# Performance work log

Hardware: AMD Instinct MI355X
Metric: run time of the kernel (lower is better)

Reference implementation:

```python
import jax, jax.numpy as jnp
import numpy as np

B, D, NH, NT = 4096, 2048, 16, 4
DK = D // NH
EPS = 1e-5


def setup_inputs() -> dict:
    key = jax.random.key(0)
    ks = jax.random.split(key, 16)
    s = 0.02
    inp = {
        "e0": jax.random.normal(ks[0], (B, D), jnp.float32),
        "e1": jax.random.normal(ks[1], (B, D), jnp.float32),
        "e2": jax.random.normal(ks[2], (B, D), jnp.float32),
        "e3": jax.random.normal(ks[3], (B, D), jnp.float32),
        "quality": jax.random.uniform(ks[4], (B, NT), jnp.float32),
        "Wq": jax.random.normal(ks[5], (D, D), jnp.float32) * s,
        "bq": jnp.zeros((D,), jnp.float32),
        "Wk": jax.random.normal(ks[6], (D, D), jnp.float32) * s,
        "bk": jnp.zeros((D,), jnp.float32),
        "Wv": jax.random.normal(ks[7], (D, D), jnp.float32) * s,
        "bv": jnp.zeros((D,), jnp.float32),
        "Wo": jax.random.normal(ks[8], (D, D), jnp.float32) * s,
        "bo": jnp.zeros((D,), jnp.float32),
        "gamma": jnp.ones((D,), jnp.float32),
        "beta": jnp.zeros((D,), jnp.float32),
    }
    return inp


def _layer_norm(x, gamma, beta):
    mu = jnp.mean(x, axis=-1, keepdims=True)
    var = jnp.mean(jnp.square(x - mu), axis=-1, keepdims=True)
    return (x - mu) * jax.lax.rsqrt(var + EPS) * gamma + beta


def reference(e0, e1, e2, e3, quality, Wq, bq, Wk, bk, Wv, bv, Wo, bo, gamma, beta):
    # H: (B, T=4, D) stacked evidence representations
    H = jnp.stack([e0, e1, e2, e3], axis=1)
    # QKV projections, reshaped to (B, heads, T, dk)
    def proj(W, b):
        return (jnp.einsum('btd,ed->bte', H, W) + b).reshape(B, NT, NH, DK).transpose(0, 2, 1, 3)
    Q, K, V = proj(Wq, bq), proj(Wk, bk), proj(Wv, bv)
    # scores: (B, heads, Tq, Tk), scaled then multiplicatively quality-gated on keys
    scores = jnp.einsum('bhid,bhjd->bhij', Q, K) / jnp.sqrt(jnp.float32(DK))
    scores = scores * quality[:, None, None, :]
    attn = jax.nn.softmax(scores, axis=-1)  # dropout = identity at inference
    ctx = jnp.einsum('bhij,bhjd->bhid', attn, V)          # (B, H, T, dk)
    ctx = ctx.transpose(0, 2, 1, 3).reshape(B, NT, D)      # (B, T, D)
    ctx = jnp.einsum('btd,ed->bte', ctx, Wo) + bo
    fused = jnp.mean(ctx, axis=1)       # mean over evidence types
    residual = jnp.mean(H, axis=1)      # mean of ALL evidence types
    return _layer_norm(fused + residual, gamma, beta)
```

## Files before the change

### kernel.cpp

```cpp
#include <hip/hip_runtime.h>
#include <cstdint>
#include <cstddef>

#define BB 4096
#define DD 2048
#define NHH 16
#define NTT 4
#define DKK 128

using u16 = unsigned short;
using u32 = unsigned int;

typedef __bf16 bf16x8 __attribute__((ext_vector_type(8)));
typedef float f32x4 __attribute__((ext_vector_type(4)));

__device__ __forceinline__ float b2f(u16 u) {
    union { float f; u32 i; } c; c.i = ((u32)u) << 16; return c.f;
}
__device__ __forceinline__ u16 f2b(float f) {
    union { float f; u32 i; } c; c.f = f;
    u32 x = c.i;
    u32 r = (x + 0x7fffu + ((x >> 16) & 1u)) >> 16;
    return (u16)r;
}
__device__ __forceinline__ u32 pk(float lo, float hi) {
    u32 a = __builtin_bit_cast(u32, lo) + 0x8000u;
    u32 b = __builtin_bit_cast(u32, hi) + 0x8000u;
    return __builtin_amdgcn_perm(b, a, 0x07060302u);
}

__device__ __forceinline__ void load_lds16(const void* g, void* l) {
    __builtin_amdgcn_global_load_lds((const __attribute__((address_space(1))) void*)g,
                                     (__attribute__((address_space(3))) void*)l,
                                     16, 0, 0);
}

__global__ __launch_bounds__(256) void cvt_all(
    const float* __restrict__ e0, const float* __restrict__ e1,
    const float* __restrict__ e2, const float* __restrict__ e3,
    const float* __restrict__ Wq, const float* __restrict__ Wk,
    const float* __restrict__ Wv, const float* __restrict__ Wo,
    u16* __restrict__ Ebf, u16* __restrict__ W4, float* __restrict__ resid)
{
    const int blk = blockIdx.x;
    const int tid = threadIdx.x;
    if (blk < 4096) {
        const int b = blk;
        const int c = tid * 8;
        const size_t rb = (size_t)b * DD + c;
        const float* eps[4] = {e0, e1, e2, e3};
        float a8[8] = {0, 0, 0, 0, 0, 0, 0, 0};
#pragma unroll
        for (int t = 0; t < 4; ++t) {
            float4 p0 = *(const float4*)(eps[t] + rb);
            float4 p1 = *(const float4*)(eps[t] + rb + 4);
            u16* dst = Ebf + ((size_t)(b * 4 + t)) * DD + c;
            *(uint4*)dst = make_uint4(pk(p0.x, p0.y), pk(p0.z, p0.w),
                                      pk(p1.x, p1.y), pk(p1.z, p1.w));
            a8[0] += p0.x; a8[1] += p0.y; a8[2] += p0.z; a8[3] += p0.w;
            a8[4] += p1.x; a8[5] += p1.y; a8[6] += p1.z; a8[7] += p1.w;
        }
        *(float4*)(resid + rb)     = make_float4(a8[0] * 0.25f, a8[1] * 0.25f,
                                                 a8[2] * 0.25f, a8[3] * 0.25f);
        *(float4*)(resid + rb + 4) = make_float4(a8[4] * 0.25f, a8[5] * 0.25f,
                                                 a8[6] * 0.25f, a8[7] * 0.25f);
    } else {
        const int wb = blk - 4096;
        const int w = wb >> 11;
        const float* src = (w == 0) ? Wq : (w == 1) ? Wk : (w == 2) ? Wv : Wo;
        u16* dst = W4 + (size_t)w * DD * DD;
        const size_t i = (size_t)(wb & 2047) * 2048 + tid * 8;
        float4 a = *(const float4*)(src + i);
        float4 c2 = *(const float4*)(src + i + 4);
        *(uint4*)(dst + i) = make_uint4(pk(a.x, a.y), pk(a.z, a.w),
                                        pk(c2.x, c2.y), pk(c2.z, c2.w));
    }
}

__global__ __launch_bounds__(256, 2) void qkv_attn(
    const u16* __restrict__ Ebf,
    const u16* __restrict__ Wqb, const u16* __restrict__ Wkb,
    const u16* __restrict__ Wvb,
    const float* __restrict__ bq, const float* __restrict__ bk,
    const float* __restrict__ bv, const float* __restrict__ qual,
    u16* __restrict__ ctx)
{
    __shared__ __align__(16) u16 As [128 * 64];
    __shared__ __align__(16) u16 BQs[128 * 64];
    __shared__ __align__(16) u16 BKs[128 * 64];
    __shared__ __align__(16) u16 BVs[128 * 64];
    __shared__ float exch[4][4][4][16];

    const int tid = threadIdx.x;
    const int h = blockIdx.x;
    const int m0 = blockIdx.y * 128;
    const int n0 = h * 128;

    const int wave = tid >> 6;
    const int lane = tid & 63;

    const int srow = wave * 8 + (lane >> 3);
    const int scol = ((lane & 7) ^ (lane >> 3)) * 8;
    const u16* srcA = Ebf + (size_t)(m0 + srow) * DD + scol;
    const u16* srcQ = Wqb + (size_t)(n0 + srow) * DD + scol;
    const u16* srcK = Wkb + (size_t)(n0 + srow) * DD + scol;
    const u16* srcV = Wvb + (size_t)(n0 + srow) * DD + scol;

    char* ldsA = (char*)As  + wave * 1024;
    char* ldsQ = (char*)BQs + wave * 1024;
    char* ldsK = (char*)BKs + wave * 1024;
    char* ldsV = (char*)BVs + wave * 1024;

    const int lrow = lane & 15;
    const int q4 = lane >> 4;
    const int wm = (wave >> 1) * 64;
    const int wn = (wave & 1) * 64;
    const int soff0 = (q4 ^ (lrow & 7)) * 16;

    f32x4 aQ[4][4] = {};
    f32x4 aK[4][4] = {};
    f32x4 aV[4][4] = {};

    for (int k0 = 0; k0 < DD; k0 += 64) {
        __syncthreads();
#pragma unroll
        for (int i = 0; i < 4; ++i) {
            const size_t go = (size_t)i * 32 * DD;
            load_lds16(srcA + go, ldsA + i * 4096);
            load_lds16(srcQ + go, ldsQ + i * 4096);
            load_lds16(srcK + go, ldsK + i * 4096);
            load_lds16(srcV + go, ldsV + i * 4096);
        }
        srcA += 64; srcQ += 64; srcK += 64; srcV += 64;
        __syncthreads();

#pragma unroll
        for (int kk = 0; kk < 2; ++kk) {
            const int so = soff0 ^ (kk * 64);
            bf16x8 af[4];
#pragma unroll
            for (int mi = 0; mi < 4; ++mi)
                af[mi] = *(const bf16x8*)((const char*)As + (wm + mi * 16 + lrow) * 128 + so);
            {
                bf16x8 b4[4];
#pragma unroll
                for (int ni = 0; ni < 4; ++ni)
                    b4[ni] = *(const bf16x8*)((const char*)BQs + (wn + ni * 16 + lrow) * 128 + so);
#pragma unroll
                for (int mi = 0; mi < 4; ++mi)
#pragma unroll
                    for (int ni = 0; ni < 4; ++ni)
                        aQ[mi][ni] = __builtin_amdgcn_mfma_f32_16x16x32_bf16(af[mi], b4[ni], aQ[mi][ni], 0, 0, 0);
            }
            __builtin_amdgcn_sched_barrier(0);
            {
                bf16x8 b4[4];
#pragma unroll
                for (int ni = 0; ni < 4; ++ni)
                    b4[ni] = *(const bf16x8*)((const char*)BKs + (wn + ni * 16 + lrow) * 128 + so);
#pragma unroll
                for (int mi = 0; mi < 4; ++mi)
#pragma unroll
                    for (int ni = 0; ni < 4; ++ni)
                        aK[mi][ni] = __builtin_amdgcn_mfma_f32_16x16x32_bf16(af[mi], b4[ni], aK[mi][ni], 0, 0, 0);
            }
            __builtin_amdgcn_sched_barrier(0);
            {
                bf16x8 b4[4];
#pragma unroll
                for (int ni = 0; ni < 4; ++ni)
                    b4[ni] = *(const bf16x8*)((const char*)BVs + (wn + ni * 16 + lrow) * 128 + so);
#pragma unroll
                for (int mi = 0; mi < 4; ++mi)
#pragma unroll
                    for (int ni = 0; ni < 4; ++ni)
                        aV[mi][ni] = __builtin_amdgcn_mfma_f32_16x16x32_bf16(af[mi], b4[ni], aV[mi][ni], 0, 0, 0);
            }
            __builtin_amdgcn_sched_barrier(0);
        }
    }

    const int quad = lane >> 4;
    const int lcol = lane & 15;

    float qb[4], kb[4], vb[4];
#pragma unroll
    for (int ni = 0; ni < 4; ++ni) {
        const int col = n0 + wn + ni * 16 + lcol;
        qb[ni] = bq[col]; kb[ni] = bk[col]; vb[ni] = bv[col];
    }

#pragma unroll
    for (int mi = 0; mi < 4; ++mi) {
        float ps[4][4];
#pragma unroll
        for (int t = 0; t < 4; ++t)
#pragma unroll
            for (int j = 0; j < 4; ++j) ps[t][j] = 0.f;

#pragma unroll
        for (int ni = 0; ni < 4; ++ni) {
            float qv[4], kv[4];
#pragma unroll
            for (int t = 0; t < 4; ++t) {
                qv[t] = aQ[mi][ni][t] + qb[ni];
                kv[t] = aK[mi][ni][t] + kb[ni];
            }
#pragma unroll
            for (int t = 0; t < 4; ++t)
#pragma unroll
                for (int j = 0; j < 4; ++j) ps[t][j] += qv[t] * kv[j];
        }
#pragma unroll
        for (int t = 0; t < 4; ++t)
#pragma unroll
            for (int j = 0; j < 4; ++j) {
                ps[t][j] += __shfl_xor(ps[t][j], 1);
                ps[t][j] += __shfl_xor(ps[t][j], 2);
                ps[t][j] += __shfl_xor(ps[t][j], 4);
                ps[t][j] += __shfl_xor(ps[t][j], 8);
            }
        if (lcol == 0) {
#pragma unroll
            for (int t = 0; t < 4; ++t)
#pragma unroll
                for (int j = 0; j < 4; ++j)
                    exch[wave][mi][quad][t * 4 + j] = ps[t][j];
        }
    }
    __syncthreads();

    const float scale = 0.08838834764831845f;
#pragma unroll
    for (int mi = 0; mi < 4; ++mi) {
        const int bbat = (m0 >> 2) + (wave >> 1) * 16 + mi * 4 + quad;

        float s16[16];
#pragma unroll
        for (int v = 0; v < 16; ++v)
            s16[v] = exch[wave][mi][quad][v] + exch[wave ^ 1][mi][quad][v];

        float qj[4];
#pragma unroll
        for (int j = 0; j < 4; ++j) qj[j] = qual[bbat * 4 + j] * scale;

        float wsum[4] = {0.f, 0.f, 0.f, 0.f};
#pragma unroll
        for (int t = 0; t < 4; ++t) {
            float sm[4]; float mx = -1e30f;
#pragma unroll
            for (int j = 0; j < 4; ++j) { sm[j] = s16[t * 4 + j] * qj[j]; mx = fmaxf(mx, sm[j]); }
            float ex[4]; float se = 0.f;
#pragma unroll
            for (int j = 0; j < 4; ++j) { ex[j] = __expf(sm[j] - mx); se += ex[j]; }
            const float inv = 0.25f / se;
#pragma unroll
            for (int j = 0; j < 4; ++j) wsum[j] += ex[j] * inv;
        }

#pragma unroll
        for (int ni = 0; ni < 4; ++ni) {
            const int col = n0 + wn + ni * 16 + lcol;
            float r = wsum[0] * aV[mi][ni][0] + wsum[1] * aV[mi][ni][1]
                    + wsum[2] * aV[mi][ni][2] + wsum[3] * aV[mi][ni][3] + vb[ni];
            ctx[(size_t)bbat * DD + col] = f2b(r);
        }
    }
}

__global__ __launch_bounds__(256) void o_gemm(
    const u16* __restrict__ A, const u16* __restrict__ W,
    const float* __restrict__ bia, float* __restrict__ Y)
{
    __shared__ __align__(16) u16 As[128 * 64];
    __shared__ __align__(16) u16 Bs[128 * 64];

    const int tid = threadIdx.x;
    const int m0 = blockIdx.x * 128;
    const int n0 = blockIdx.y * 128;

    const int wave = tid >> 6;
    const int lane = tid & 63;

    const int srow = wave * 8 + (lane >> 3);
    const int scol = ((lane & 7) ^ (lane >> 3)) * 8;
    const u16* srcA = A + (size_t)(m0 + srow) * DD + scol;
    const u16* srcB = W + (size_t)(n0 + srow) * DD + scol;

    char* ldsA = (char*)As + wave * 1024;
    char* ldsB = (char*)Bs + wave * 1024;

    const int wm = (wave >> 1) * 64;
    const int wn = (wave & 1) * 64;
    const int lrow = lane & 15;
    const int q4 = lane >> 4;
    const int soff0 = (q4 ^ (lrow & 7)) * 16;

    f32x4 acc[4][4] = {};

    for (int k0 = 0; k0 < DD; k0 += 64) {
        __syncthreads();
#pragma unroll
        for (int i = 0; i < 4; ++i) {
            const size_t go = (size_t)i * 32 * DD;
            load_lds16(srcA + go, ldsA + i * 4096);
            load_lds16(srcB + go, ldsB + i * 4096);
        }
        srcA += 64; srcB += 64;
        __syncthreads();

#pragma unroll
        for (int kk = 0; kk < 2; ++kk) {
            const int so = soff0 ^ (kk * 64);
            bf16x8 af[4], bfr[4];
#pragma unroll
            for (int i = 0; i < 4; ++i)
                af[i] = *(const bf16x8*)((const char*)As + (wm + i * 16 + lrow) * 128 + so);
#pragma unroll
            for (int i = 0; i < 4; ++i)
                bfr[i] = *(const bf16x8*)((const char*)Bs + (wn + i * 16 + lrow) * 128 + so);
#pragma unroll
            for (int mi = 0; mi < 4; ++mi)
#pragma unroll
                for (int ni = 0; ni < 4; ++ni)
                    acc[mi][ni] = __builtin_amdgcn_mfma_f32_16x16x32_bf16(af[mi], bfr[ni], acc[mi][ni], 0, 0, 0);
        }
    }

#pragma unroll
    for (int mi = 0; mi < 4; ++mi) {
#pragma unroll
        for (int r = 0; r < 4; ++r) {
            const int grow = m0 + wm + mi * 16 + (lane >> 4) * 4 + r;
#pragma unroll
            for (int ni = 0; ni < 4; ++ni) {
                const int gcol = n0 + wn + ni * 16 + (lane & 15);
                Y[(size_t)grow * DD + gcol] = acc[mi][ni][r] + bia[gcol];
            }
        }
    }
}

__global__ __launch_bounds__(256) void ln_kernel(
    const float* __restrict__ Y,
    const float* __restrict__ resid,
    const float* __restrict__ gamma, const float* __restrict__ beta,
    float* __restrict__ out)
{
    const int r = blockIdx.x;
    const int tid = threadIdx.x;
    const int c = tid * 8;
    const size_t base = (size_t)r * DD + c;

    float v[8];
    {
        float4 y0 = *(const float4*)(Y + base);
        float4 y1 = *(const float4*)(Y + base + 4);
        float4 r0 = *(const float4*)(resid + base);
        float4 r1 = *(const float4*)(resid + base + 4);
        v[0] = y0.x + r0.x; v[1] = y0.y + r0.y; v[2] = y0.z + r0.z; v[3] = y0.w + r0.w;
        v[4] = y1.x + r1.x; v[5] = y1.y + r1.y; v[6] = y1.z + r1.z; v[7] = y1.w + r1.w;
    }

    float s = 0.f, sq = 0.f;
#pragma unroll
    for (int i = 0; i < 8; ++i) { s += v[i]; sq += v[i] * v[i]; }
#pragma unroll
    for (int off = 32; off >= 1; off >>= 1) {
        s += __shfl_xor(s, off);
        sq += __shfl_xor(sq, off);
    }
    __shared__ float sh[8];
    const int lane = tid & 63, wv = tid >> 6;
    if (lane == 0) { sh[wv] = s; sh[4 + wv] = sq; }
    __syncthreads();
    s = sh[0] + sh[1] + sh[2] + sh[3];
    sq = sh[4] + sh[5] + sh[6] + sh[7];

    const float invD = 1.0f / 2048.0f;
    const float mu = s * invD;
    const float rs = rsqrtf(sq * invD - mu * mu + 1e-5f);

    float4 g0 = *(const float4*)(gamma + c);
    float4 g1 = *(const float4*)(gamma + c + 4);
    float4 b0 = *(const float4*)(beta + c);
    float4 b1 = *(const float4*)(beta + c + 4);
    float gg[8] = {g0.x, g0.y, g0.z, g0.w, g1.x, g1.y, g1.z, g1.w};
    float bb[8] = {b0.x, b0.y, b0.z, b0.w, b1.x, b1.y, b1.z, b1.w};

    float o[8];
#pragma unroll
    for (int i = 0; i < 8; ++i) o[i] = (v[i] - mu) * rs * gg[i] + bb[i];
    *(float4*)(out + base)     = make_float4(o[0], o[1], o[2], o[3]);
    *(float4*)(out + base + 4) = make_float4(o[4], o[5], o[6], o[7]);
}

extern "C" void kernel_launch(void* const* d_in, const int* in_sizes, int n_in,
                              void* d_out, int out_size, void* d_ws, size_t ws_size,
                              hipStream_t stream)
{
    const float* e0   = (const float*)d_in[0];
    const float* e1   = (const float*)d_in[1];
    const float* e2   = (const float*)d_in[2];
    const float* e3   = (const float*)d_in[3];
    const float* qual = (const float*)d_in[4];
    const float* Wq   = (const float*)d_in[5];
    const float* bq   = (const float*)d_in[6];
    const float* Wk   = (const float*)d_in[7];
    const float* bk   = (const float*)d_in[8];
    const float* Wv   = (const float*)d_in[9];
    const float* bv   = (const float*)d_in[10];
    const float* Wo   = (const float*)d_in[11];
    const float* bo   = (const float*)d_in[12];
    const float* gm   = (const float*)d_in[13];
    const float* bt   = (const float*)d_in[14];

    const size_t WD = (size_t)DD * DD;
    const size_t MQ = (size_t)BB * NTT * DD;
    const size_t ED = (size_t)BB * DD;

    u16* Ebf = (u16*)d_ws;
    u16* W4  = Ebf + MQ;
    u16* ctx = W4 + 4 * WD;
    float* Y = (float*)(ctx + ED);
    float* resid = Y + ED;

    cvt_all<<<dim3(12288), 256, 0, stream>>>(e0, e1, e2, e3, Wq, Wk, Wv, Wo,
                                             Ebf, W4, resid);

    qkv_attn<<<dim3(16, 128), 256, 0, stream>>>(Ebf, W4, W4 + WD, W4 + 2 * WD,
                                                bq, bk, bv, qual, ctx);

    o_gemm<<<dim3(32, 16), 256, 0, stream>>>(ctx, W4 + 3 * WD, bo, Y);

    ln_kernel<<<dim3(4096), 256, 0, stream>>>(Y, resid, gm, bt,
                                              (float*)d_out);
}
```

Measured before the change: 621.6 us.

## Double-buffer LDS tiles with K=32 stages in QKV and output GEMMs

Both GEMM kernels switch from a single 64-wide K tile, loaded and then computed between two barriers, to two 32-wide K buffers in LDS. The next stage's global-to-LDS loads are issued before computing on the current buffer, so memory latency overlaps with MFMA work and each K step needs one barrier instead of two. The LDS swizzle is changed to match 64-byte rows. LDS footprint stays the same, but each stage carries half as much work per barrier, and correctness depends on the async loads completing before the barrier.

Result: slower. 686.9 us (+10.5%).

```diff
diff --git a/kernel.cpp b/kernel.cpp
--- a/kernel.cpp
+++ b/kernel.cpp
@@ -77,6 +77,70 @@
     }
 }
 
+#define QKV_COMPUTE(BI)                                                        \
+    {                                                                          \
+        bf16x8 af[4];                                                          \
+        _Pragma("unroll")                                                      \
+        for (int mi = 0; mi < 4; ++mi)                                         \
+            af[mi] = *(const bf16x8*)((const char*)As[BI] +                    \
+                     (wm + mi * 16 + lrow) * 64 + soff);                       \
+        {                                                                      \
+            bf16x8 b4[4];                                                      \
+            _Pragma("unroll")                                                  \
+            for (int ni = 0; ni < 4; ++ni)                                     \
+                b4[ni] = *(const bf16x8*)((const char*)BQs[BI] +               \
+                         (wn + ni * 16 + lrow) * 64 + soff);                   \
+            _Pragma("unroll")                                                  \
+            for (int mi = 0; mi < 4; ++mi)                                     \
+                _Pragma("unroll")                                              \
+                for (int ni = 0; ni < 4; ++ni)                                 \
+                    aQ[mi][ni] = __builtin_amdgcn_mfma_f32_16x16x32_bf16(      \
+                        af[mi], b4[ni], aQ[mi][ni], 0, 0, 0);                  \
+        }                                                                      \
+        __builtin_amdgcn_sched_barrier(0);                                     \
+        {                                                                      \
+            bf16x8 b4[4];                                                      \
+            _Pragma("unroll")                                                  \
+            for (int ni = 0; ni < 4; ++ni)                                     \
+                b4[ni] = *(const bf16x8*)((const char*)BKs[BI] +               \
+                         (wn + ni * 16 + lrow) * 64 + soff);                   \
+            _Pragma("unroll")                                                  \
+            for (int mi = 0; mi < 4; ++mi)                                     \
+                _Pragma("unroll")                                              \
+                for (int ni = 0; ni < 4; ++ni)                                 \
+                    aK[mi][ni] = __builtin_amdgcn_mfma_f32_16x16x32_bf16(      \
+                        af[mi], b4[ni], aK[mi][ni], 0, 0, 0);                  \
+        }                                                                      \
+        __builtin_amdgcn_sched_barrier(0);                                     \
+        {                                                                      \
+            bf16x8 b4[4];                                                      \
+            _Pragma("unroll")                                                  \
+            for (int ni = 0; ni < 4; ++ni)                                     \
+                b4[ni] = *(const bf16x8*)((const char*)BVs[BI] +               \
+                         (wn + ni * 16 + lrow) * 64 + soff);                   \
+            _Pragma("unroll")                                                  \
+            for (int mi = 0; mi < 4; ++mi)                                     \
+                _Pragma("unroll")                                              \
+                for (int ni = 0; ni < 4; ++ni)                                 \
+                    aV[mi][ni] = __builtin_amdgcn_mfma_f32_16x16x32_bf16(      \
+                        af[mi], b4[ni], aV[mi][ni], 0, 0, 0);                  \
+        }                                                                      \
+        __builtin_amdgcn_sched_barrier(0);                                     \
+    }
+
+#define QKV_STAGE(BI, KT)                                                      \
+    {                                                                          \
+        const size_t ko = (size_t)(KT) * 32;                                   \
+        char* dA = (char*)As[BI]  + wave * 1024;                               \
+        char* dQ = (char*)BQs[BI] + wave * 1024;                               \
+        char* dK = (char*)BKs[BI] + wave * 1024;                               \
+        char* dV = (char*)BVs[BI] + wave * 1024;                               \
+        load_lds16(srcA + ko, dA);       load_lds16(srcA + ko + D64, dA + 4096);\
+        load_lds16(srcQ + ko, dQ);       load_lds16(srcQ + ko + D64, dQ + 4096);\
+        load_lds16(srcK + ko, dK);       load_lds16(srcK + ko + D64, dK + 4096);\
+        load_lds16(srcV + ko, dV);       load_lds16(srcV + ko + D64, dV + 4096);\
+    }
+
 __global__ __launch_bounds__(256, 2) void qkv_attn(
     const u16* __restrict__ Ebf,
     const u16* __restrict__ Wqb, const u16* __restrict__ Wkb,
@@ -85,10 +149,10 @@
     const float* __restrict__ bv, const float* __restrict__ qual,
     u16* __restrict__ ctx)
 {
-    __shared__ __align__(16) u16 As [128 * 64];
-    __shared__ __align__(16) u16 BQs[128 * 64];
-    __shared__ __align__(16) u16 BKs[128 * 64];
-    __shared__ __align__(16) u16 BVs[128 * 64];
+    __shared__ __align__(16) u16 As [2][128 * 32];
+    __shared__ __align__(16) u16 BQs[2][128 * 32];
+    __shared__ __align__(16) u16 BKs[2][128 * 32];
+    __shared__ __align__(16) u16 BVs[2][128 * 32];
     __shared__ float exch[4][4][4][16];
 
     const int tid = threadIdx.x;
@@ -99,85 +163,35 @@
     const int wave = tid >> 6;
     const int lane = tid & 63;
 
-    const int srow = wave * 8 + (lane >> 3);
-    const int scol = ((lane & 7) ^ (lane >> 3)) * 8;
+    const int srow = wave * 16 + (lane >> 2);
+    const int scol = ((lane & 3) ^ ((lane >> 3) & 3)) * 8;
     const u16* srcA = Ebf + (size_t)(m0 + srow) * DD + scol;
     const u16* srcQ = Wqb + (size_t)(n0 + srow) * DD + scol;
     const u16* srcK = Wkb + (size_t)(n0 + srow) * DD + scol;
     const u16* srcV = Wvb + (size_t)(n0 + srow) * DD + scol;
-
-    char* ldsA = (char*)As  + wave * 1024;
-    char* ldsQ = (char*)BQs + wave * 1024;
-    char* ldsK = (char*)BKs + wave * 1024;
-    char* ldsV = (char*)BVs + wave * 1024;
+    const size_t D64 = (size_t)64 * DD;
 
     const int lrow = lane & 15;
     const int q4 = lane >> 4;
     const int wm = (wave >> 1) * 64;
     const int wn = (wave & 1) * 64;
-    const int soff0 = (q4 ^ (lrow & 7)) * 16;
+    const int soff = (q4 ^ ((lrow >> 1) & 3)) * 16;
 
     f32x4 aQ[4][4] = {};
     f32x4 aK[4][4] = {};
     f32x4 aV[4][4] = {};
 
-    for (int k0 = 0; k0 < DD; k0 += 64) {
+    QKV_STAGE(0, 0);
+    __syncthreads();
+
+#pragma unroll 1
+    for (int it = 0; it < 64; it += 2) {
+        QKV_STAGE(1, it + 1);
+        QKV_COMPUTE(0);
         __syncthreads();
-#pragma unroll
-        for (int i = 0; i < 4; ++i) {
-            const size_t go = (size_t)i * 32 * DD;
-            load_lds16(srcA + go, ldsA + i * 4096);
-            load_lds16(srcQ + go, ldsQ + i * 4096);
-            load_lds16(srcK + go, ldsK + i * 4096);
-            load_lds16(srcV + go, ldsV + i * 4096);
-        }
-        srcA += 64; srcQ += 64; srcK += 64; srcV += 64;
+        if (it + 2 < 64) QKV_STAGE(0, it + 2);
+        QKV_COMPUTE(1);
         __syncthreads();
-
-#pragma unroll
-        for (int kk = 0; kk < 2; ++kk) {
-            const int so = soff0 ^ (kk * 64);
-            bf16x8 af[4];
-#pragma unroll
-            for (int mi = 0; mi < 4; ++mi)
-                af[mi] = *(const bf16x8*)((const char*)As + (wm + mi * 16 + lrow) * 128 + so);
-            {
-                bf16x8 b4[4];
-#pragma unroll
-                for (int ni = 0; ni < 4; ++ni)
-                    b4[ni] = *(const bf16x8*)((const char*)BQs + (wn + ni * 16 + lrow) * 128 + so);
-#pragma unroll
-                for (int mi = 0; mi < 4; ++mi)
-#pragma unroll
-                    for (int ni = 0; ni < 4; ++ni)
-                        aQ[mi][ni] = __builtin_amdgcn_mfma_f32_16x16x32_bf16(af[mi], b4[ni], aQ[mi][ni], 0, 0, 0);
-            }
-            __builtin_amdgcn_sched_barrier(0);
-            {
-                bf16x8 b4[4];
-#pragma unroll
-                for (int ni = 0; ni < 4; ++ni)
-                    b4[ni] = *(const bf16x8*)((const char*)BKs + (wn + ni * 16 + lrow) * 128 + so);
-#pragma unroll
-                for (int mi = 0; mi < 4; ++mi)
-#pragma unroll
-                    for (int ni = 0; ni < 4; ++ni)
-                        aK[mi][ni] = __builtin_amdgcn_mfma_f32_16x16x32_bf16(af[mi], b4[ni], aK[mi][ni], 0, 0, 0);
-            }
-            __builtin_amdgcn_sched_barrier(0);
-            {
-                bf16x8 b4[4];
-#pragma unroll
-                for (int ni = 0; ni < 4; ++ni)
-                    b4[ni] = *(const bf16x8*)((const char*)BVs + (wn + ni * 16 + lrow) * 128 + so);
-#pragma unroll
-                for (int mi = 0; mi < 4; ++mi)
-#pragma unroll
-                    for (int ni = 0; ni < 4; ++ni)
-                        aV[mi][ni] = __builtin_amdgcn_mfma_f32_16x16x32_bf16(af[mi], b4[ni], aV[mi][ni], 0, 0, 0);
-            }
-            __builtin_amdgcn_sched_barrier(0);
-        }
     }
 
     const int quad = lane >> 4;
@@ -268,12 +282,40 @@
     }
 }
 
+#define O_STAGE(BI, KT)                                                        \
+    {                                                                          \
+        const size_t ko = (size_t)(KT) * 32;                                   \
+        char* dA = (char*)As[BI] + wave * 1024;                                \
+        char* dB = (char*)Bs[BI] + wave * 1024;                                \
+        load_lds16(srcA + ko, dA);      load_lds16(srcA + ko + D64, dA + 4096);\
+        load_lds16(srcB + ko, dB);      load_lds16(srcB + ko + D64, dB + 4096);\
+    }
+
+#define O_COMPUTE(BI)                                                          \
+    {                                                                          \
+        bf16x8 af[4], bfr[4];                                                  \
+        _Pragma("unroll")                                                      \
+        for (int i = 0; i < 4; ++i)                                            \
+            af[i] = *(const bf16x8*)((const char*)As[BI] +                     \
+                    (wm + i * 16 + lrow) * 64 + soff);                         \
+        _Pragma("unroll")                                                      \
+        for (int i = 0; i < 4; ++i)                                            \
+            bfr[i] = *(const bf16x8*)((const char*)Bs[BI] +                    \
+                     (wn + i * 16 + lrow) * 64 + soff);                        \
+        _Pragma("unroll")                                                      \
+        for (int mi = 0; mi < 4; ++mi)                                         \
+            _Pragma("unroll")                                                  \
+            for (int ni = 0; ni < 4; ++ni)                                     \
+                acc[mi][ni] = __builtin_amdgcn_mfma_f32_16x16x32_bf16(         \
+                    af[mi], bfr[ni], acc[mi][ni], 0, 0, 0);                    \
+    }
+
 __global__ __launch_bounds__(256) void o_gemm(
     const u16* __restrict__ A, const u16* __restrict__ W,
     const float* __restrict__ bia, float* __restrict__ Y)
 {
-    __shared__ __align__(16) u16 As[128 * 64];
-    __shared__ __align__(16) u16 Bs[128 * 64];
+    __shared__ __align__(16) u16 As[2][128 * 32];
+    __shared__ __align__(16) u16 Bs[2][128 * 32];
 
     const int tid = threadIdx.x;
     const int m0 = blockIdx.x * 128;
@@ -282,49 +324,31 @@
     const int wave = tid >> 6;
     const int lane = tid & 63;
 
-    const int srow = wave * 8 + (lane >> 3);
-    const int scol = ((lane & 7) ^ (lane >> 3)) * 8;
+    const int srow = wave * 16 + (lane >> 2);
+    const int scol = ((lane & 3) ^ ((lane >> 3) & 3)) * 8;
     const u16* srcA = A + (size_t)(m0 + srow) * DD + scol;
     const u16* srcB = W + (size_t)(n0 + srow) * DD + scol;
-
-    char* ldsA = (char*)As + wave * 1024;
-    char* ldsB = (char*)Bs + wave * 1024;
+    const size_t D64 = (size_t)64 * DD;
 
     const int wm = (wave >> 1) * 64;
     const int wn = (wave & 1) * 64;
     const int lrow = lane & 15;
     const int q4 = lane >> 4;
-    const int soff0 = (q4 ^ (lrow & 7)) * 16;
+    const int soff = (q4 ^ ((lrow >> 1) & 3)) * 16;
 
     f32x4 acc[4][4] = {};
 
-    for (int k0 = 0; k0 < DD; k0 += 64) {
+    O_STAGE(0, 0);
+    __syncthreads();
+
+#pragma unroll 1
+    for (int it = 0; it < 64; it += 2) {
+        O_STAGE(1, it + 1);
+        O_COMPUTE(0);
         __syncthreads();
-#pragma unroll
-        for (int i = 0; i < 4; ++i) {
-            const size_t go = (size_t)i * 32 * DD;
-            load_lds16(srcA + go, ldsA + i * 4096);
-            load_lds16(srcB + go, ldsB + i * 4096);
-        }
-        srcA += 64; srcB += 64;
+        if (it + 2 < 64) O_STAGE(0, it + 2);
+        O_COMPUTE(1);
         __syncthreads();
-
-#pragma unroll
-        for (int kk = 0; kk < 2; ++kk) {
-            const int so = soff0 ^ (kk * 64);
-            bf16x8 af[4], bfr[4];
-#pragma unroll
-            for (int i = 0; i < 4; ++i)
-                af[i] = *(const bf16x8*)((const char*)As + (wm + i * 16 + lrow) * 128 + so);
-#pragma unroll
-            for (int i = 0; i < 4; ++i)
-                bfr[i] = *(const bf16x8*)((const char*)Bs + (wn + i * 16 + lrow) * 128 + so);
-#pragma unroll
-            for (int mi = 0; mi < 4; ++mi)
-#pragma unroll
-                for (int ni = 0; ni < 4; ++ni)
-                    acc[mi][ni] = __builtin_amdgcn_mfma_f32_16x16x32_bf16(af[mi], bfr[ni], acc[mi][ni], 0, 0, 0);
-        }
     }
 
 #pragma unroll
```
